# Performance work log

Hardware: AMD Instinct MI355X
Metric: run time of the kernel (lower is better)

The kernel has to match this reference:

```python
import jax, jax.numpy as jnp
import numpy as np

GROUP_SIZE = 64
SCALING = 1.0  # lora_alpha / r = 16 / 16
# bitsandbytes NF4 codebook (16 normal-float levels)
NF4_CODE = jnp.array([
    -1.0, -0.6961928009986877, -0.5250730514526367, -0.39491748809814453,
    -0.28444138169288635, -0.18477343022823334, -0.09105003625154495, 0.0,
    0.07958029955625534, 0.16093020141124725, 0.24611230194568634,
    0.33791524171829224, 0.44070982933044434, 0.5626170039176941,
    0.7229568362236023, 1.0], dtype=jnp.float32)

IN_F, OUT_F, R, TOKENS = 4096, 11008, 16, 32


def setup_inputs() -> dict:
    key = jax.random.key(0)
    k0, k1, k2, k3, k4 = jax.random.split(key, 5)
    x = jax.random.normal(k0, (TOKENS, IN_F), dtype=jnp.float32)
    # each byte packs two 4-bit NF4 indices (high nibble first)
    packed_weight = jax.random.randint(k1, (OUT_F * IN_F // 2,), 0, 256, dtype=jnp.int32)
    # per-group absmax scales (positive)
    scales = jax.random.uniform(k2, (OUT_F * IN_F // GROUP_SIZE,), dtype=jnp.float32,
                                minval=0.005, maxval=0.05)
    lora_A = jax.random.normal(k3, (R, IN_F), dtype=jnp.float32) * 0.02
    lora_B = jax.random.normal(k4, (OUT_F, R), dtype=jnp.float32) * 0.02
    return {"x": x, "packed_weight": packed_weight, "scales": scales,
            "lora_A": lora_A, "lora_B": lora_B}


def _dequant_nf4(packed_weight, scales):
    hi = packed_weight // 16          # first nibble
    lo = packed_weight % 16           # second nibble
    idx = jnp.stack([hi, lo], axis=-1).reshape(-1)          # [out*in]
    w = NF4_CODE[idx].reshape(-1, GROUP_SIZE) * scales[:, None]
    return w.reshape(OUT_F, IN_F)                            # [out, in]


def reference(x, packed_weight, scales, lora_A, lora_B):
    W = _dequant_nf4(packed_weight, scales)
    base = x @ W.T                                           # [tokens, out]
    lora = (x @ lora_A.T) @ lora_B.T                         # low-rank update
    return base + SCALING * lora
```

## Files before the change

kernel.cpp:

```cpp
#include <hip/hip_runtime.h>
#include <hip/hip_bf16.h>

#define IN_F 4096
#define OUT_F 11008
#define TOKENS 32
#define RANK 16
#define KSPLIT 8
#define KSLICE (IN_F / KSPLIT)
#define XPAD 520

typedef unsigned short u16;
typedef __attribute__((ext_vector_type(8))) short bf16x8;
typedef __attribute__((ext_vector_type(4))) float f32x4;

__device__ const float NF4_d[16] = {
    -1.0f, -0.6961928009986877f, -0.5250730514526367f, -0.39491748809814453f,
    -0.28444138169288635f, -0.18477343022823334f, -0.09105003625154495f, 0.0f,
    0.07958029955625534f, 0.16093020141124725f, 0.24611230194568634f,
    0.33791524171829224f, 0.44070982933044434f, 0.5626170039176941f,
    0.7229568362236023f, 1.0f};

static __device__ __forceinline__ unsigned pk2(float a, float b) {
    __hip_bfloat162 h = __float22bfloat162_rn(make_float2(a, b));
    unsigned u;
    __builtin_memcpy(&u, &h, 4);
    return u;
}

__global__ void prep(const float* __restrict__ x, const float* __restrict__ A,
                     u16* __restrict__ xbf, float* __restrict__ xa) {
    __shared__ float red[256];
    if (blockIdx.x >= 512) {
        int i4 = (blockIdx.x - 512) * 256 + threadIdx.x;
        float4 v = ((const float4*)x)[i4];
        uint2 o;
        o.x = pk2(v.x, v.y);
        o.y = pk2(v.z, v.w);
        ((uint2*)xbf)[i4] = o;
        return;
    }
    int b = blockIdx.x;
    int t = b >> 4, r = b & 15;
    const float4* xr = (const float4*)(x + t * IN_F);
    const float4* ar = (const float4*)(A + r * IN_F);
    float s = 0.f;
    for (int c = 0; c < 4; ++c) {
        int j = c * 256 + threadIdx.x;
        float4 xv = xr[j], av = ar[j];
        s += xv.x * av.x + xv.y * av.y + xv.z * av.z + xv.w * av.w;
    }
    red[threadIdx.x] = s;
    __syncthreads();
    for (int st = 128; st > 0; st >>= 1) {
        if (threadIdx.x < st) red[threadIdx.x] += red[threadIdx.x + st];
        __syncthreads();
    }
    if (threadIdx.x == 0) xa[b] = red[0];
}

__global__ void lora_out(const float* __restrict__ xa, const float* __restrict__ B,
                         float* __restrict__ out) {
    int idx4 = blockIdx.x * 256 + threadIdx.x;
    int t = idx4 / (OUT_F / 4);
    int o4 = idx4 - t * (OUT_F / 4);
    const float4* br = (const float4*)(B + o4 * 4 * RANK);
    const float4* xr = (const float4*)(xa + t * RANK);
    float4 xv0 = xr[0], xv1 = xr[1], xv2 = xr[2], xv3 = xr[3];
    float res[4];
#pragma unroll
    for (int j = 0; j < 4; ++j) {
        float4 b0 = br[j * 4 + 0], b1 = br[j * 4 + 1];
        float4 b2 = br[j * 4 + 2], b3 = br[j * 4 + 3];
        res[j] = b0.x * xv0.x + b0.y * xv0.y + b0.z * xv0.z + b0.w * xv0.w +
                 b1.x * xv1.x + b1.y * xv1.y + b1.z * xv1.z + b1.w * xv1.w +
                 b2.x * xv2.x + b2.y * xv2.y + b2.z * xv2.z + b2.w * xv2.w +
                 b3.x * xv3.x + b3.y * xv3.y + b3.z * xv3.z + b3.w * xv3.w;
    }
    float4 r4 = make_float4(res[0], res[1], res[2], res[3]);
    *(float4*)(out + t * OUT_F + o4 * 4) = r4;
}

__global__ __launch_bounds__(256, 4) void qlora_main(const int* __restrict__ packed,
                                                     const float* __restrict__ scales,
                                                     const u16* __restrict__ xbf,
                                                     float* __restrict__ out) {
    __shared__ u16 xs[32 * XPAD];
    __shared__ unsigned tbl[256];
    const int tid = threadIdx.x;
    const int kbase = blockIdx.y * KSLICE;
    const int obase = blockIdx.x * 64;

    const int lane = tid & 63;
    const int wv = tid >> 6;
    const int n = lane & 15;
    const int q = lane >> 4;
    const int o = obase + wv * 16 + n;

    const int4* ppq = (const int4*)(packed + o * 2048 + (kbase >> 1)) + q;
    int4 P0 = ppq[0];
    int4 P1 = ppq[4];
    int4 P2 = ppq[8];
    int4 P3 = ppq[12];

    const float4* sp = (const float4*)(scales + o * 64 + (kbase >> 6));
    float4 sA = sp[0], sB = sp[1];

    tbl[tid] = pk2(NF4_d[tid & 15], NF4_d[tid >> 4]);

    for (int it = 0; it < 8; ++it) {
        int row = it * 4 + (tid >> 6);
        int c8 = tid & 63;
        *(uint4*)(xs + row * XPAD + c8 * 8) =
            *(const uint4*)(xbf + row * IN_F + kbase + c8 * 8);
    }
    __syncthreads();

    f32x4 acc0 = {0.f, 0.f, 0.f, 0.f};
    f32x4 acc1 = {0.f, 0.f, 0.f, 0.f};
    const u16* xr0 = xs + n * XPAD + q * 8;
    const u16* xr1 = xs + (n + 16) * XPAD + q * 8;

    int4 P[4] = {P0, P1, P2, P3};
    const float scr[8] = {sA.x, sA.y, sA.z, sA.w, sB.x, sB.y, sB.z, sB.w};

#pragma unroll
    for (int s = 0; s < 16; ++s) {
        int4 cur = P[s & 3];
        if (s + 4 < 16) P[s & 3] = ppq[(s + 4) * 4];
        float sc = scr[s >> 1];

        unsigned u0 = tbl[cur.x & 255];
        unsigned u1 = tbl[cur.y & 255];
        unsigned u2 = tbl[cur.z & 255];
        unsigned u3 = tbl[cur.w & 255];
        uint4 bu;
        {
            float h = __int_as_float(u0 & 0xFFFF0000u);
            float l = __int_as_float(u0 << 16);
            bu.x = pk2(h * sc, l * sc);
        }
        {
            float h = __int_as_float(u1 & 0xFFFF0000u);
            float l = __int_as_float(u1 << 16);
            bu.y = pk2(h * sc, l * sc);
        }
        {
            float h = __int_as_float(u2 & 0xFFFF0000u);
            float l = __int_as_float(u2 << 16);
            bu.z = pk2(h * sc, l * sc);
        }
        {
            float h = __int_as_float(u3 & 0xFFFF0000u);
            float l = __int_as_float(u3 << 16);
            bu.w = pk2(h * sc, l * sc);
        }
        bf16x8 bfrag;
        __builtin_memcpy(&bfrag, &bu, 16);
        bf16x8 a0 = *(const bf16x8*)(xr0 + s * 32);
        bf16x8 a1 = *(const bf16x8*)(xr1 + s * 32);
        acc0 = __builtin_amdgcn_mfma_f32_16x16x32_bf16(a0, bfrag, acc0, 0, 0, 0);
        acc1 = __builtin_amdgcn_mfma_f32_16x16x32_bf16(a1, bfrag, acc1, 0, 0, 0);
    }

    for (int r = 0; r < 4; ++r) {
        int t = q * 4 + r;
        atomicAdd(out + t * OUT_F + o, acc0[r]);
        atomicAdd(out + (t + 16) * OUT_F + o, acc1[r]);
    }
}

extern "C" void kernel_launch(void* const* d_in, const int* in_sizes, int n_in,
                              void* d_out, int out_size, void* d_ws, size_t ws_size,
                              hipStream_t stream) {
    const float* x = (const float*)d_in[0];
    const int* packed = (const int*)d_in[1];
    const float* scales = (const float*)d_in[2];
    const float* lora_A = (const float*)d_in[3];
    const float* lora_B = (const float*)d_in[4];
    float* out = (float*)d_out;

    u16* xbf = (u16*)d_ws;
    float* xa = (float*)((char*)d_ws + 262144);

    prep<<<640, 256, 0, stream>>>(x, lora_A, xbf, xa);
    lora_out<<<(TOKENS * OUT_F / 4) / 256, 256, 0, stream>>>(xa, lora_B, out);
    qlora_main<<<dim3(OUT_F / 64, KSPLIT), 256, 0, stream>>>(packed, scales, xbf, out);
}
```

Before: 158.5 us.

## Fuse LoRA output and x bf16 conversion into main kernel, zero output in prep

Drops the separate lora_out kernel. The k-slice-0 blocks now compute the LoRA contribution from xa and B and add it into their atomic adds, while the prep kernel only zeroes the output. The fp32 to bf16 conversion of x moves into the main kernel's shared-memory staging, so the xbf workspace round trip goes away, and packed-weight loads become nontemporal. This saves one launch and some global traffic, but every main block now reads fp32 x, which doubles the x bytes per block, and the zero pass still writes the whole output.

```diff
diff --git a/kernel.cpp b/kernel.cpp
--- a/kernel.cpp
+++ b/kernel.cpp
@@ -8,10 +8,12 @@
 #define KSPLIT 8
 #define KSLICE (IN_F / KSPLIT)
 #define XPAD 520
+#define OUT_ELEMS (TOKENS * OUT_F)
 
 typedef unsigned short u16;
 typedef __attribute__((ext_vector_type(8))) short bf16x8;
 typedef __attribute__((ext_vector_type(4))) float f32x4;
+typedef __attribute__((ext_vector_type(4))) int i32x4;
 
 __device__ const float NF4_d[16] = {
     -1.0f, -0.6961928009986877f, -0.5250730514526367f, -0.39491748809814453f,
@@ -27,16 +29,13 @@
     return u;
 }
 
-__global__ void prep(const float* __restrict__ x, const float* __restrict__ A,
-                     u16* __restrict__ xbf, float* __restrict__ xa) {
+__global__ void prep_xa_zero(const float* __restrict__ x, const float* __restrict__ A,
+                             float* __restrict__ xa, float* __restrict__ out) {
     __shared__ float red[256];
     if (blockIdx.x >= 512) {
-        int i4 = (blockIdx.x - 512) * 256 + threadIdx.x;
-        float4 v = ((const float4*)x)[i4];
-        uint2 o;
-        o.x = pk2(v.x, v.y);
-        o.y = pk2(v.z, v.w);
-        ((uint2*)xbf)[i4] = o;
+        int i = (blockIdx.x - 512) * 256 + threadIdx.x;
+        float4 z = make_float4(0.f, 0.f, 0.f, 0.f);
+        for (int j = i; j < OUT_ELEMS / 4; j += 16384) ((float4*)out)[j] = z;
         return;
     }
     int b = blockIdx.x;
@@ -58,34 +57,13 @@
     if (threadIdx.x == 0) xa[b] = red[0];
 }
 
-__global__ void lora_out(const float* __restrict__ xa, const float* __restrict__ B,
-                         float* __restrict__ out) {
-    int idx4 = blockIdx.x * 256 + threadIdx.x;
-    int t = idx4 / (OUT_F / 4);
-    int o4 = idx4 - t * (OUT_F / 4);
-    const float4* br = (const float4*)(B + o4 * 4 * RANK);
-    const float4* xr = (const float4*)(xa + t * RANK);
-    float4 xv0 = xr[0], xv1 = xr[1], xv2 = xr[2], xv3 = xr[3];
-    float res[4];
-#pragma unroll
-    for (int j = 0; j < 4; ++j) {
-        float4 b0 = br[j * 4 + 0], b1 = br[j * 4 + 1];
-        float4 b2 = br[j * 4 + 2], b3 = br[j * 4 + 3];
-        res[j] = b0.x * xv0.x + b0.y * xv0.y + b0.z * xv0.z + b0.w * xv0.w +
-                 b1.x * xv1.x + b1.y * xv1.y + b1.z * xv1.z + b1.w * xv1.w +
-                 b2.x * xv2.x + b2.y * xv2.y + b2.z * xv2.z + b2.w * xv2.w +
-                 b3.x * xv3.x + b3.y * xv3.y + b3.z * xv3.z + b3.w * xv3.w;
-    }
-    float4 r4 = make_float4(res[0], res[1], res[2], res[3]);
-    *(float4*)(out + t * OUT_F + o4 * 4) = r4;
-}
-
-__global__ __launch_bounds__(256, 4) void qlora_main(const int* __restrict__ packed,
-                                                     const float* __restrict__ scales,
-                                                     const u16* __restrict__ xbf,
-                                                     float* __restrict__ out) {
+__global__ __launch_bounds__(256, 4) void qlora_fused(
+    const int* __restrict__ packed, const float* __restrict__ scales,
+    const float* __restrict__ x, const float* __restrict__ xa,
+    const float* __restrict__ B, float* __restrict__ out) {
     __shared__ u16 xs[32 * XPAD];
     __shared__ unsigned tbl[256];
+    __shared__ float xal[512];
     const int tid = threadIdx.x;
     const int kbase = blockIdx.y * KSLICE;
     const int obase = blockIdx.x * 64;
@@ -96,22 +74,34 @@
     const int q = lane >> 4;
     const int o = obase + wv * 16 + n;
 
-    const int4* ppq = (const int4*)(packed + o * 2048 + (kbase >> 1)) + q;
-    int4 P0 = ppq[0];
-    int4 P1 = ppq[4];
-    int4 P2 = ppq[8];
-    int4 P3 = ppq[12];
+    const i32x4* ppq = (const i32x4*)(packed + o * 2048 + (kbase >> 1)) + q;
+    i32x4 P[4];
+    P[0] = __builtin_nontemporal_load(ppq);
+    P[1] = __builtin_nontemporal_load(ppq + 4);
+    P[2] = __builtin_nontemporal_load(ppq + 8);
+    P[3] = __builtin_nontemporal_load(ppq + 12);
 
     const float4* sp = (const float4*)(scales + o * 64 + (kbase >> 6));
     float4 sA = sp[0], sB = sp[1];
 
     tbl[tid] = pk2(NF4_d[tid & 15], NF4_d[tid >> 4]);
 
+    if (blockIdx.y == 0) {
+        xal[tid] = xa[tid];
+        xal[tid + 256] = xa[tid + 256];
+    }
+
     for (int it = 0; it < 8; ++it) {
         int row = it * 4 + (tid >> 6);
         int c8 = tid & 63;
-        *(uint4*)(xs + row * XPAD + c8 * 8) =
-            *(const uint4*)(xbf + row * IN_F + kbase + c8 * 8);
+        const float4* src = (const float4*)(x + row * IN_F + kbase + c8 * 8);
+        float4 v0 = src[0], v1 = src[1];
+        uint4 d;
+        d.x = pk2(v0.x, v0.y);
+        d.y = pk2(v0.z, v0.w);
+        d.z = pk2(v1.x, v1.y);
+        d.w = pk2(v1.z, v1.w);
+        *(uint4*)(xs + row * XPAD + c8 * 8) = d;
     }
     __syncthreads();
 
@@ -119,41 +109,23 @@
     f32x4 acc1 = {0.f, 0.f, 0.f, 0.f};
     const u16* xr0 = xs + n * XPAD + q * 8;
     const u16* xr1 = xs + (n + 16) * XPAD + q * 8;
-
-    int4 P[4] = {P0, P1, P2, P3};
     const float scr[8] = {sA.x, sA.y, sA.z, sA.w, sB.x, sB.y, sB.z, sB.w};
 
 #pragma unroll
     for (int s = 0; s < 16; ++s) {
-        int4 cur = P[s & 3];
-        if (s + 4 < 16) P[s & 3] = ppq[(s + 4) * 4];
+        i32x4 cur = P[s & 3];
+        if (s + 4 < 16) P[s & 3] = __builtin_nontemporal_load(ppq + (s + 4) * 4);
         float sc = scr[s >> 1];
 
-        unsigned u0 = tbl[cur.x & 255];
-        unsigned u1 = tbl[cur.y & 255];
-        unsigned u2 = tbl[cur.z & 255];
-        unsigned u3 = tbl[cur.w & 255];
+        unsigned u0 = tbl[cur[0] & 255];
+        unsigned u1 = tbl[cur[1] & 255];
+        unsigned u2 = tbl[cur[2] & 255];
+        unsigned u3 = tbl[cur[3] & 255];
         uint4 bu;
-        {
-            float h = __int_as_float(u0 & 0xFFFF0000u);
-            float l = __int_as_float(u0 << 16);
-            bu.x = pk2(h * sc, l * sc);
-        }
-        {
-            float h = __int_as_float(u1 & 0xFFFF0000u);
-            float l = __int_as_float(u1 << 16);
-            bu.y = pk2(h * sc, l * sc);
-        }
-        {
-            float h = __int_as_float(u2 & 0xFFFF0000u);
-            float l = __int_as_float(u2 << 16);
-            bu.z = pk2(h * sc, l * sc);
-        }
-        {
-            float h = __int_as_float(u3 & 0xFFFF0000u);
-            float l = __int_as_float(u3 << 16);
-            bu.w = pk2(h * sc, l * sc);
-        }
+        bu.x = pk2(__int_as_float(u0 & 0xFFFF0000u) * sc, __int_as_float(u0 << 16) * sc);
+        bu.y = pk2(__int_as_float(u1 & 0xFFFF0000u) * sc, __int_as_float(u1 << 16) * sc);
+        bu.z = pk2(__int_as_float(u2 & 0xFFFF0000u) * sc, __int_as_float(u2 << 16) * sc);
+        bu.w = pk2(__int_as_float(u3 & 0xFFFF0000u) * sc, __int_as_float(u3 << 16) * sc);
         bf16x8 bfrag;
         __builtin_memcpy(&bfrag, &bu, 16);
         bf16x8 a0 = *(const bf16x8*)(xr0 + s * 32);
@@ -162,10 +134,37 @@
         acc1 = __builtin_amdgcn_mfma_f32_16x16x32_bf16(a1, bfrag, acc1, 0, 0, 0);
     }
 
+    float lora[8] = {0.f, 0.f, 0.f, 0.f, 0.f, 0.f, 0.f, 0.f};
+    if (blockIdx.y == 0) {
+        const float4* br = (const float4*)(B + o * RANK);
+        float4 b0 = br[0], b1 = br[1], b2 = br[2], b3 = br[3];
+#pragma unroll
+        for (int r = 0; r < 4; ++r) {
+            const float* x0 = xal + (q * 4 + r) * RANK;
+            const float* x1 = xal + (q * 4 + r + 16) * RANK;
+            float s0 = 0.f, s1 = 0.f;
+#pragma unroll
+            for (int j = 0; j < 4; ++j) {
+                const float4 bj = ((const float4*)&b0)[0];
+            }
+            s0 = b0.x * x0[0] + b0.y * x0[1] + b0.z * x0[2] + b0.w * x0[3] +
+                 b1.x * x0[4] + b1.y * x0[5] + b1.z * x0[6] + b1.w * x0[7] +
+                 b2.x * x0[8] + b2.y * x0[9] + b2.z * x0[10] + b2.w * x0[11] +
+                 b3.x * x0[12] + b3.y * x0[13] + b3.z * x0[14] + b3.w * x0[15];
+            s1 = b0.x * x1[0] + b0.y * x1[1] + b0.z * x1[2] + b0.w * x1[3] +
+                 b1.x * x1[4] + b1.y * x1[5] + b1.z * x1[6] + b1.w * x1[7] +
+                 b2.x * x1[8] + b2.y * x1[9] + b2.z * x1[10] + b2.w * x1[11] +
+                 b3.x * x1[12] + b3.y * x1[13] + b3.z * x1[14] + b3.w * x1[15];
+            lora[r] = s0;
+            lora[r + 4] = s1;
+        }
+    }
+
+#pragma unroll
     for (int r = 0; r < 4; ++r) {
         int t = q * 4 + r;
-        atomicAdd(out + t * OUT_F + o, acc0[r]);
-        atomicAdd(out + (t + 16) * OUT_F + o, acc1[r]);
+        atomicAdd(out + t * OUT_F + o, acc0[r] + lora[r]);
+        atomicAdd(out + (t + 16) * OUT_F + o, acc1[r] + lora[r + 4]);
     }
 }
 
@@ -179,10 +178,9 @@
     const float* lora_B = (const float*)d_in[4];
     float* out = (float*)d_out;
 
-    u16* xbf = (u16*)d_ws;
-    float* xa = (float*)((char*)d_ws + 262144);
+    float* xa = (float*)d_ws;
 
-    prep<<<640, 256, 0, stream>>>(x, lora_A, xbf, xa);
-    lora_out<<<(TOKENS * OUT_F / 4) / 256, 256, 0, stream>>>(xa, lora_B, out);
-    qlora_main<<<dim3(OUT_F / 64, KSPLIT), 256, 0, stream>>>(packed, scales, xbf, out);
+    prep_xa_zero<<<576, 256, 0, stream>>>(x, lora_A, xa, out);
+    qlora_fused<<<dim3(OUT_F / 64, KSPLIT), 256, 0, stream>>>(packed, scales, x, xa,
+                                                              lora_B, out);
 }
```

After: 152.7 us. 3.7% less time.
